# Performance work log

Hardware: AMD Instinct MI355X
Metric: run time of the kernel (lower is better)

## Reference

```python
import jax, jax.numpy as jnp
import numpy as np

B, S, H = 8, 1024, 768
NH, DH = 12, 64
F, E = 3072, 8
EPS = 1e-12

def layer_norm(x, g, b):
    mu = jnp.mean(x, axis=-1, keepdims=True)
    var = jnp.var(x, axis=-1, keepdims=True)
    return g * (x - mu) / jnp.sqrt(var + EPS) + b

def setup_inputs():
    key = jax.random.key(0)
    ks = jax.random.split(key, 20)
    std = 0.02
    d = {
        'hidden_states': jax.random.normal(ks[0], (B, S, H), jnp.float32),
        'Wq': jax.random.normal(ks[1], (H, H)) * std, 'bq': jnp.zeros((H,)),
        'Wk': jax.random.normal(ks[2], (H, H)) * std, 'bk': jnp.zeros((H,)),
        'Wv': jax.random.normal(ks[3], (H, H)) * std, 'bv': jnp.zeros((H,)),
        'Wao': jax.random.normal(ks[4], (H, H)) * std, 'bao': jnp.zeros((H,)),
        'ln1_g': jnp.ones((H,)), 'ln1_b': jnp.zeros((H,)),
        'Wr': jax.random.normal(ks[5], (H, E)) * std, 'br': jnp.zeros((E,)),
        'Wi': jax.random.normal(ks[6], (E, H, F)) * std, 'bi': jnp.zeros((E, F)),
        'Wo': jax.random.normal(ks[7], (F, H)) * std, 'bo': jnp.zeros((H,)),
        'ln2_g': jnp.ones((H,)), 'ln2_b': jnp.zeros((H,)),
    }
    return d

def reference(hidden_states, Wq, bq, Wk, bk, Wv, bv, Wao, bao, ln1_g, ln1_b,
              Wr, br, Wi, bi, Wo, bo, ln2_g, ln2_b):
    b, s, h = hidden_states.shape
    # --- self attention ---
    q = (hidden_states @ Wq + bq).reshape(b, s, NH, DH)
    k = (hidden_states @ Wk + bk).reshape(b, s, NH, DH)
    v = (hidden_states @ Wv + bv).reshape(b, s, NH, DH)
    scores = jnp.einsum('bqhd,bkhd->bhqk', q, k) / jnp.sqrt(jnp.float32(DH))
    probs = jax.nn.softmax(scores, axis=-1)
    ctx = jnp.einsum('bhqk,bkhd->bqhd', probs, v).reshape(b, s, h)
    attention_output = layer_norm(ctx @ Wao + bao + hidden_states, ln1_g, ln1_b)
    # --- router ---
    routing_scores = jax.nn.softmax(attention_output @ Wr + br, axis=-1)  # [b,s,E]
    routing_expert = jnp.argmax(routing_scores, axis=-1)  # [b,s]
    # --- expert FFN (dispatch/combine via per-expert masking) ---
    flat_x = attention_output.reshape(-1, h)          # [T,H]
    flat_e = routing_expert.reshape(-1)               # [T]
    flat_inter = jnp.zeros((b * s, F), flat_x.dtype)
    for e in range(E):
        mask = (flat_e == e)[:, None].astype(flat_x.dtype)
        y = jax.nn.gelu(flat_x @ Wi[e] + bi[e], approximate=False)
        flat_inter = flat_inter + mask * y
    inter = flat_inter.reshape(b, s, F)
    # --- output (dense + residual layernorm) ---
    layer_output = layer_norm(inter @ Wo + bo + attention_output, ln2_g, ln2_b)
    return layer_output, routing_scores
```

## Files before the change

kernel.cpp:

```cpp
#include <hip/hip_runtime.h>
#include <math.h>
#include <stdint.h>

#define TOKS 8192
#define HDIM 768
#define FDIM 3072
#define NEXP 8
#define NHEAD 12
#define SEQ 1024
#define BATCH 8
#define PERMSZ 9216

typedef __attribute__((ext_vector_type(8))) short s16x8;
typedef __attribute__((ext_vector_type(4))) short s16x4;
typedef __attribute__((ext_vector_type(4))) float f32x4;

__device__ __forceinline__ short f2bf(float f) {
  uint32_t u = __float_as_uint(f);
  uint32_t r = (u + 0x7fffu + ((u >> 16) & 1u)) >> 16;
  return (short)(r & 0xffffu);
}
__device__ __forceinline__ float bf2f(short h) {
  return __uint_as_float(((uint32_t)(uint16_t)h) << 16);
}
__device__ __forceinline__ void gload16(const void* g, void* l) {
  __builtin_amdgcn_global_load_lds(
      (const __attribute__((address_space(1))) uint32_t*)g,
      (__attribute__((address_space(3))) uint32_t*)l, 16, 0, 0);
}
__device__ __forceinline__ void pipe_wait_barrier() {
  asm volatile("s_waitcnt vmcnt(0)" ::: "memory");
  __builtin_amdgcn_s_barrier();
}

__global__ __launch_bounds__(256) void convert_split(
    const float* __restrict__ X, short* __restrict__ Xh, short* __restrict__ Xl, int n4)
{
  const int i = blockIdx.x * 256 + threadIdx.x;
  if (i >= n4) return;
  const float4 v = ((const float4*)X)[i];
  const float a[4] = {v.x, v.y, v.z, v.w};
  s16x4 h, l;
#pragma unroll
  for (int j = 0; j < 4; ++j) {
    h[j] = f2bf(a[j]);
    l[j] = f2bf(a[j] - bf2f(h[j]));
  }
  ((s16x4*)Xh)[i] = h;
  ((s16x4*)Xl)[i] = l;
}

__global__ __launch_bounds__(256) void transpose_split(
    const float* __restrict__ W, short* __restrict__ WTh, short* __restrict__ WTl,
    int K, int N)
{
  __shared__ float t[32][33];
  const int tid = threadIdx.x;
  const int tx = tid & 31, ty = tid >> 5;
  const int n0 = blockIdx.x * 32, k0 = blockIdx.y * 32;
#pragma unroll
  for (int r = 0; r < 4; ++r)
    t[ty + r * 8][tx] = W[(size_t)(k0 + ty + r * 8) * N + n0 + tx];
  __syncthreads();
#pragma unroll
  for (int r = 0; r < 4; ++r) {
    const float v = t[tx][ty + r * 8];
    const short h = f2bf(v);
    WTh[(size_t)(n0 + ty + r * 8) * K + k0 + tx] = h;
    WTl[(size_t)(n0 + ty + r * 8) * K + k0 + tx] = f2bf(v - bf2f(h));
  }
}

__global__ __launch_bounds__(256) void qkv_split_mfma(
    const short* __restrict__ Ah, const short* __restrict__ Al,
    const short* __restrict__ BhT, const short* __restrict__ BlT,
    const float* __restrict__ bias,
    short* __restrict__ QKh, short* __restrict__ QKl,
    short* __restrict__ VTh, short* __restrict__ VTl)
{
  const int K = 768;
  __shared__ __align__(16) short lAh[4096];
  __shared__ __align__(16) short lAl[4096];
  __shared__ __align__(16) short lBh[2][4096];
  __shared__ __align__(16) short lBl[2][4096];
  const int dsp = blockIdx.x + 18 * blockIdx.y;
  const int orig = (dsp & 7) * 144 + (dsp >> 3);
  const int bx = orig % 18, by = orig / 18;
  const int tid = threadIdx.x;
  const int w = tid >> 6, lane = tid & 63;
  const int wr = w >> 1, wc = w & 1;
  const int row0 = by * 128, col0 = bx * 128;
  const int sr = lane & 15, kg = lane >> 4;
  const size_t a0 = (size_t)(row0 + 2 * w * 16 + sr) * K + kg * 8;
  const size_t a1 = a0 + (size_t)16 * K;
  const size_t b0 = (size_t)(col0 + 2 * w * 16 + sr) * K + kg * 8;
  const size_t b1 = b0 + (size_t)16 * K;
  const int d0 = (2 * w) * 512, d1 = (2 * w + 1) * 512;
#define STAGE_QA(k0) do { \
    gload16(Ah + a0 + (k0), &lAh[d0]); \
    gload16(Ah + a1 + (k0), &lAh[d1]); \
    gload16(Al + a0 + (k0), &lAl[d0]); \
    gload16(Al + a1 + (k0), &lAl[d1]); \
  } while (0)
#define STAGE_QB(bu, k0) do { \
    gload16(BhT + b0 + (k0), &lBh[bu][d0]); \
    gload16(BhT + b1 + (k0), &lBh[bu][d1]); \
    gload16(BlT + b0 + (k0), &lBl[bu][d0]); \
    gload16(BlT + b1 + (k0), &lBl[bu][d1]); \
  } while (0)
  f32x4 acc[4][4] = {};
  STAGE_QA(0);
  STAGE_QB(0, 0);
  pipe_wait_barrier();
  int cur = 0;
  for (int t = 0; t < 24; ++t) {
    s16x8 ah[4], al[4], bh[4], bl[4];
#pragma unroll
    for (int i = 0; i < 4; ++i) {
      ah[i] = *(const s16x8*)&lAh[(wr * 4 + i) * 512 + lane * 8];
      al[i] = *(const s16x8*)&lAl[(wr * 4 + i) * 512 + lane * 8];
      bh[i] = *(const s16x8*)&lBh[cur][(wc * 4 + i) * 512 + lane * 8];
      bl[i] = *(const s16x8*)&lBl[cur][(wc * 4 + i) * 512 + lane * 8];
    }
    __syncthreads();
    if (t < 23) {
      STAGE_QA((t + 1) * 32);
      STAGE_QB(cur ^ 1, (t + 1) * 32);
    }
#pragma unroll
    for (int mi = 0; mi < 4; ++mi)
#pragma unroll
      for (int ni = 0; ni < 4; ++ni) {
        acc[mi][ni] = __builtin_amdgcn_mfma_f32_16x16x32_bf16(ah[mi], bh[ni], acc[mi][ni], 0, 0, 0);
        acc[mi][ni] = __builtin_amdgcn_mfma_f32_16x16x32_bf16(ah[mi], bl[ni], acc[mi][ni], 0, 0, 0);
        acc[mi][ni] = __builtin_amdgcn_mfma_f32_16x16x32_bf16(al[mi], bh[ni], acc[mi][ni], 0, 0, 0);
      }
    pipe_wait_barrier();
    cur ^= 1;
  }
#undef STAGE_QA
#undef STAGE_QB
  const int cl = lane & 15, rg = lane >> 4;
#pragma unroll
  for (int mi = 0; mi < 4; ++mi)
#pragma unroll
    for (int ni = 0; ni < 4; ++ni) {
      const int c = col0 + wc * 64 + ni * 16 + cl;
      const int rowb = row0 + wr * 64 + mi * 16 + rg * 4;
      const float qscale = (c < 768) ? 0.125f : 1.0f;
      s16x4 hv, lv;
#pragma unroll
      for (int r = 0; r < 4; ++r) {
        const float v = (acc[mi][ni][r] + bias[c]) * qscale;
        const short hh = f2bf(v);
        hv[r] = hh;
        lv[r] = f2bf(v - bf2f(hh));
      }
      if (c < 1536) {
#pragma unroll
        for (int r = 0; r < 4; ++r) {
          QKh[(size_t)(rowb + r) * 1536 + c] = hv[r];
          QKl[(size_t)(rowb + r) * 1536 + c] = lv[r];
        }
      } else {
        const int dall = c - 1536;
        const size_t vi = (((size_t)((rowb >> 10) * NHEAD + (dall >> 6))) * 64 + (dall & 63)) * 1024
                          + (rowb & 1023);
        *(s16x4*)(VTh + vi) = hv;
        *(s16x4*)(VTl + vi) = lv;
      }
    }
}

__global__ __launch_bounds__(256) void gemm_splitk_staged(
    const short* __restrict__ Ah, const short* __restrict__ Al,
    const short* __restrict__ BhT, const short* __restrict__ BlT,
    const float* __restrict__ bias, float* __restrict__ C0, float* __restrict__ C1,
    int N, int K)
{
  __shared__ __align__(16) short lAh[2][4096];
  __shared__ __align__(16) short lAl[2][4096];
  __shared__ __align__(16) short lBh[2][4096];
  __shared__ __align__(16) short lBl[2][4096];
  const int tid = threadIdx.x;
  const int w = tid >> 6, lane = tid & 63;
  const int wr = w >> 1, wc = w & 1;
  const int row0 = blockIdx.y * 128, col0 = blockIdx.x * 128;
  const int z = blockIdx.z;
  const int Khalf = K >> 1, koff = z * Khalf;
  const int sr = lane & 15, kg = lane >> 4;
  const size_t a0 = (size_t)(row0 + 2 * w * 16 + sr) * K + koff + kg * 8;
  const size_t a1 = a0 + (size_t)16 * K;
  const size_t b0 = (size_t)(col0 + 2 * w * 16 + sr) * K + koff + kg * 8;
  const size_t b1 = b0 + (size_t)16 * K;
  const int d0 = (2 * w) * 512, d1 = (2 * w + 1) * 512;
#define STAGE_K4(bu, k0) do { \
    gload16(Ah + a0 + (k0), &lAh[bu][d0]); \
    gload16(Ah + a1 + (k0), &lAh[bu][d1]); \
    gload16(Al + a0 + (k0), &lAl[bu][d0]); \
    gload16(Al + a1 + (k0), &lAl[bu][d1]); \
    gload16(BhT + b0 + (k0), &lBh[bu][d0]); \
    gload16(BhT + b1 + (k0), &lBh[bu][d1]); \
    gload16(BlT + b0 + (k0), &lBl[bu][d0]); \
    gload16(BlT + b1 + (k0), &lBl[bu][d1]); \
  } while (0)
  f32x4 acc[4][4] = {};
  const int NT = Khalf >> 5;
  STAGE_K4(0, 0);
  pipe_wait_barrier();
  int cur = 0;
  for (int t = 0; t < NT; ++t) {
    if (t + 1 < NT) STAGE_K4(cur ^ 1, (t + 1) * 32);
    s16x8 ah[4], al[4], bh[4], bl[4];
#pragma unroll
    for (int i = 0; i < 4; ++i) {
      ah[i] = *(const s16x8*)&lAh[cur][(wr * 4 + i) * 512 + lane * 8];
      al[i] = *(const s16x8*)&lAl[cur][(wr * 4 + i) * 512 + lane * 8];
      bh[i] = *(const s16x8*)&lBh[cur][(wc * 4 + i) * 512 + lane * 8];
      bl[i] = *(const s16x8*)&lBl[cur][(wc * 4 + i) * 512 + lane * 8];
    }
#pragma unroll
    for (int mi = 0; mi < 4; ++mi)
#pragma unroll
      for (int ni = 0; ni < 4; ++ni) {
        acc[mi][ni] = __builtin_amdgcn_mfma_f32_16x16x32_bf16(ah[mi], bh[ni], acc[mi][ni], 0, 0, 0);
        acc[mi][ni] = __builtin_amdgcn_mfma_f32_16x16x32_bf16(ah[mi], bl[ni], acc[mi][ni], 0, 0, 0);
        acc[mi][ni] = __builtin_amdgcn_mfma_f32_16x16x32_bf16(al[mi], bh[ni], acc[mi][ni], 0, 0, 0);
      }
    pipe_wait_barrier();
    cur ^= 1;
  }
#undef STAGE_K4
  float* C = z ? C1 : C0;
  const int cl = lane & 15, rg = lane >> 4;
#pragma unroll
  for (int mi = 0; mi < 4; ++mi)
#pragma unroll
    for (int r = 0; r < 4; ++r) {
      const int row = row0 + wr * 64 + mi * 16 + rg * 4 + r;
#pragma unroll
      for (int ni = 0; ni < 4; ++ni) {
        const int c = col0 + wc * 64 + ni * 16 + cl;
        C[(size_t)row * N + c] = acc[mi][ni][r] + (z ? 0.f : bias[c]);
      }
    }
}

__global__ __launch_bounds__(128, 2) void attention_part(
    const short* __restrict__ QKh, const short* __restrict__ QKl,
    const short* __restrict__ VTh, const short* __restrict__ VTl,
    float* __restrict__ O0, float* __restrict__ O1,
    float2* __restrict__ ml0, float2* __restrict__ ml1)
{
  __shared__ __align__(16) short lPh[2][2560];
  const int tid = threadIdx.x;
  const int w = tid >> 6, lane = tid & 63;
  const int dsp = blockIdx.x + 32 * (blockIdx.y + 12 * blockIdx.z);
  const int orig = (dsp & 7) * 384 + (dsp >> 3);
  const int wx = orig & 31;
  const int b = orig / 384, h = (orig >> 5) % 12;
  const int z = wx & 1;
  const int q0 = (wx >> 1) * 64 + w * 32;
  const int kv0 = z * 512;
  const int sr = lane & 15, kg = lane >> 4;
  const int cl = sr, rg = kg;
  short* myPh = lPh[w];
  float* Op = z ? O1 : O0;
  float2* mlp = z ? ml1 : ml0;

  s16x8 qh[2][2], ql[2][2];
  {
    const size_t qbase = ((size_t)b * SEQ + q0 + sr) * 1536 + h * 64 + kg * 8;
#pragma unroll
    for (int mi = 0; mi < 2; ++mi)
#pragma unroll
      for (int ks = 0; ks < 2; ++ks) {
        const size_t o = qbase + (size_t)mi * (16 * 1536) + ks * 32;
        qh[mi][ks] = *(const s16x8*)(QKh + o);
        ql[mi][ks] = *(const s16x8*)(QKl + o);
      }
  }
  float m_run[2][4], l_run[2][4];
#pragma unroll
  for (int mi = 0; mi < 2; ++mi)
#pragma unroll
    for (int r = 0; r < 4; ++r) { m_run[mi][r] = -3.0e38f; l_run[mi][r] = 0.f; }
  f32x4 acc_o[2][4] = {};

  for (int kt = kv0; kt < kv0 + 512; kt += 64) {
    s16x8 kh[4][2];
    {
      const size_t kbase = ((size_t)b * SEQ + kt + sr) * 1536 + 768 + h * 64 + kg * 8;
#pragma unroll
      for (int ni = 0; ni < 4; ++ni)
#pragma unroll
        for (int ks = 0; ks < 2; ++ks) {
          const size_t o = kbase + (size_t)ni * (16 * 1536) + ks * 32;
          kh[ni][ks] = *(const s16x8*)(QKh + o);
        }
    }
    f32x4 accs[2][4] = {};
    __builtin_amdgcn_s_setprio(1);
#pragma unroll
    for (int ks = 0; ks < 2; ++ks)
#pragma unroll
      for (int ni = 0; ni < 4; ++ni)
#pragma unroll
        for (int mi = 0; mi < 2; ++mi) {
          accs[mi][ni] = __builtin_amdgcn_mfma_f32_16x16x32_bf16(qh[mi][ks], kh[ni][ks], accs[mi][ni], 0, 0, 0);
          accs[mi][ni] = __builtin_amdgcn_mfma_f32_16x16x32_bf16(ql[mi][ks], kh[ni][ks], accs[mi][ni], 0, 0, 0);
        }
    __builtin_amdgcn_s_setprio(0);
    s16x8 vh[4][2], vl2[4][2];
    {
      const size_t vbase = (((size_t)(b * NHEAD + h)) * 64 + sr) * 1024 + kt + kg * 8;
#pragma unroll
      for (int nd = 0; nd < 4; ++nd)
#pragma unroll
        for (int ks2 = 0; ks2 < 2; ++ks2) {
          const size_t o = vbase + (size_t)nd * (16 * 1024) + ks2 * 32;
          vh[nd][ks2] = *(const s16x8*)(VTh + o);
          vl2[nd][ks2] = *(const s16x8*)(VTl + o);
        }
    }
#pragma unroll
    for (int mi = 0; mi < 2; ++mi)
#pragma unroll
      for (int r = 0; r < 4; ++r) {
        float mx = fmaxf(fmaxf(accs[mi][0][r], accs[mi][1][r]),
                         fmaxf(accs[mi][2][r], accs[mi][3][r]));
        mx = fmaxf(mx, __shfl_xor(mx, 1));
        mx = fmaxf(mx, __shfl_xor(mx, 2));
        mx = fmaxf(mx, __shfl_xor(mx, 4));
        mx = fmaxf(mx, __shfl_xor(mx, 8));
        const float mn = fmaxf(m_run[mi][r], mx);
        const float c = __expf(m_run[mi][r] - mn);
        m_run[mi][r] = mn;
        l_run[mi][r] *= c;
#pragma unroll
        for (int nd = 0; nd < 4; ++nd) acc_o[mi][nd][r] *= c;
        float sum = 0.f;
#pragma unroll
        for (int ni = 0; ni < 4; ++ni) {
          const float p = __expf(accs[mi][ni][r] - mn);
          const short hh = f2bf(p);
          sum += bf2f(hh);
          const int idx = (mi * 2 + (ni >> 1)) * 640 + (rg * 4 + r) * 40 + (ni & 1) * 16 + cl;
          myPh[idx] = hh;
        }
        sum += __shfl_xor(sum, 1);
        sum += __shfl_xor(sum, 2);
        sum += __shfl_xor(sum, 4);
        sum += __shfl_xor(sum, 8);
        l_run[mi][r] += sum;
      }
    __builtin_amdgcn_s_setprio(1);
#pragma unroll
    for (int ks2 = 0; ks2 < 2; ++ks2) {
      s16x8 pf[2];
#pragma unroll
      for (int mi = 0; mi < 2; ++mi) {
        const int ra = (mi * 2 + ks2) * 640 + sr * 40 + kg * 8;
        pf[mi] = *(const s16x8*)&myPh[ra];
      }
#pragma unroll
      for (int nd = 0; nd < 4; ++nd)
#pragma unroll
        for (int mi = 0; mi < 2; ++mi) {
          acc_o[mi][nd] = __builtin_amdgcn_mfma_f32_16x16x32_bf16(pf[mi], vh[nd][ks2], acc_o[mi][nd], 0, 0, 0);
          acc_o[mi][nd] = __builtin_amdgcn_mfma_f32_16x16x32_bf16(pf[mi], vl2[nd][ks2], acc_o[mi][nd], 0, 0, 0);
        }
    }
    __builtin_amdgcn_s_setprio(0);
  }
#pragma unroll
  for (int mi = 0; mi < 2; ++mi)
#pragma unroll
    for (int nd = 0; nd < 4; ++nd)
#pragma unroll
      for (int r = 0; r < 4; ++r) {
        const int row = q0 + mi * 16 + rg * 4 + r;
        const int d = h * 64 + nd * 16 + cl;
        Op[((size_t)b * SEQ + row) * HDIM + d] = acc_o[mi][nd][r];
      }
  if (sr == 0) {
#pragma unroll
    for (int mi = 0; mi < 2; ++mi)
#pragma unroll
      for (int r = 0; r < 4; ++r) {
        const int row = q0 + mi * 16 + rg * 4 + r;
        mlp[(size_t)(b * NHEAD + h) * SEQ + row] = make_float2(m_run[mi][r], l_run[mi][r]);
      }
  }
}

__global__ __launch_bounds__(256) void combine_split(
    const float* __restrict__ O0, const float* __restrict__ O1,
    const float2* __restrict__ ml0, const float2* __restrict__ ml1,
    short* __restrict__ Ch, short* __restrict__ Cl)
{
  const int t = blockIdx.x;
  const int b = t >> 10, s = t & 1023;
  const int tid = threadIdx.x;
#pragma unroll
  for (int i = 0; i < 3; ++i) {
    const int idx = tid + i * 256;
    const int h = idx >> 6;
    const float2 a0 = ml0[(size_t)(b * NHEAD + h) * SEQ + s];
    const float2 a1 = ml1[(size_t)(b * NHEAD + h) * SEQ + s];
    const float mm = fmaxf(a0.x, a1.x);
    const float w0 = __expf(a0.x - mm), w1 = __expf(a1.x - mm);
    const float denom = a0.y * w0 + a1.y * w1;
    const size_t o = (size_t)t * HDIM + idx;
    const float v = (O0[o] * w0 + O1[o] * w1) / denom;
    const short hh = f2bf(v);
    Ch[o] = hh;
    Cl[o] = f2bf(v - bf2f(hh));
  }
}

__global__ __launch_bounds__(256) void transpose_to_bf16(
    const float* __restrict__ W, short* __restrict__ WT, int K, int N)
{
  const size_t off = (size_t)blockIdx.z * (size_t)K * N;
  const float* Wp = W + off;
  short* WTp = WT + off;
  __shared__ float t[32][33];
  const int tid = threadIdx.x;
  const int tx = tid & 31, ty = tid >> 5;
  const int n0 = blockIdx.x * 32, k0 = blockIdx.y * 32;
#pragma unroll
  for (int r = 0; r < 4; ++r)
    t[ty + r * 8][tx] = Wp[(size_t)(k0 + ty + r * 8) * N + n0 + tx];
  __syncthreads();
#pragma unroll
  for (int r = 0; r < 4; ++r)
    WTp[(size_t)(n0 + ty + r * 8) * K + k0 + tx] = f2bf(t[tx][ty + r * 8]);
}

__global__ __launch_bounds__(256) void expert_up_mfma(
    const short* __restrict__ Abf, const short* __restrict__ WiT,
    const float* __restrict__ bi, const int* __restrict__ perm,
    const int* __restrict__ offs, short* __restrict__ interb)
{
  const int row0 = blockIdx.x * 128;
  if (row0 >= offs[NEXP]) return;
  int e = 0;
  while (offs[e + 1] <= row0) ++e;
  __shared__ __align__(16) short lA[2][4096];
  __shared__ __align__(16) short lB[2][4096];
  __shared__ int toks[128];
  const int tid = threadIdx.x;
  const int w = tid >> 6, lane = tid & 63;
  const int wr = w >> 1, wc = w & 1;
  const int col0 = blockIdx.y * 128;
  if (tid < 128) toks[tid] = perm[row0 + tid];
  __syncthreads();
  const int sr = lane & 15, kg = lane >> 4;
  int t0 = toks[2 * w * 16 + sr];        if (t0 < 0) t0 = toks[0];
  int t1 = toks[(2 * w + 1) * 16 + sr];  if (t1 < 0) t1 = toks[0];
  const size_t a0 = (size_t)t0 * HDIM + kg * 8;
  const size_t a1 = (size_t)t1 * HDIM + kg * 8;
  const short* Bt = WiT + (size_t)e * FDIM * HDIM;
  const size_t b0 = (size_t)(col0 + 2 * w * 16 + sr) * HDIM + kg * 8;
  const size_t b1 = b0 + (size_t)16 * HDIM;
  const int d0 = (2 * w) * 512, d1 = (2 * w + 1) * 512;
#define STAGE_E(bu, k0) do { \
    gload16(Abf + a0 + (k0), &lA[bu][d0]); \
    gload16(Abf + a1 + (k0), &lA[bu][d1]); \
    gload16(Bt + b0 + (k0), &lB[bu][d0]); \
    gload16(Bt + b1 + (k0), &lB[bu][d1]); \
  } while (0)
  f32x4 acc[4][4] = {};
  STAGE_E(0, 0);
  pipe_wait_barrier();
  int cur = 0;
  for (int t = 0; t < 24; ++t) {
    if (t < 23) STAGE_E(cur ^ 1, (t + 1) * 32);
    s16x8 af[4], bg[4];
#pragma unroll
    for (int i = 0; i < 4; ++i) {
      af[i] = *(const s16x8*)&lA[cur][(wr * 4 + i) * 512 + lane * 8];
      bg[i] = *(const s16x8*)&lB[cur][(wc * 4 + i) * 512 + lane * 8];
    }
#pragma unroll
    for (int mi = 0; mi < 4; ++mi)
#pragma unroll
      for (int ni = 0; ni < 4; ++ni)
        acc[mi][ni] = __builtin_amdgcn_mfma_f32_16x16x32_bf16(af[mi], bg[ni], acc[mi][ni], 0, 0, 0);
    pipe_wait_barrier();
    cur ^= 1;
  }
#undef STAGE_E
  const int cl = lane & 15, rg = lane >> 4;
#pragma unroll
  for (int mi = 0; mi < 4; ++mi) {
#pragma unroll
    for (int r = 0; r < 4; ++r) {
      const int rl = wr * 64 + mi * 16 + rg * 4 + r;
      const int tok = toks[rl];
      if (tok < 0) continue;
#pragma unroll
      for (int ni = 0; ni < 4; ++ni) {
        const int c = col0 + wc * 64 + ni * 16 + cl;
        float v = acc[mi][ni][r] + bi[(size_t)e * FDIM + c];
        v = 0.5f * v * (1.0f + erff(v * 0.70710678118654752f));
        interb[(size_t)tok * FDIM + c] = f2bf(v);
      }
    }
  }
}

__global__ __launch_bounds__(256) void wo_mfma(
    const short* __restrict__ Ab, const short* __restrict__ BT,
    const float* __restrict__ bias, float* __restrict__ C0, float* __restrict__ C1)
{
  __shared__ __align__(16) short lA[2][4096];
  __shared__ __align__(16) short lB[2][4096];
  const int tid = threadIdx.x;
  const int w = tid >> 6, lane = tid & 63;
  const int wr = w >> 1, wc = w & 1;
  const int row0 = blockIdx.y * 128, col0 = blockIdx.x * 128;
  const int z = blockIdx.z;
  const int kbase = z * 1536;
  const int sr = lane & 15, kg = lane >> 4;
  const size_t a0 = (size_t)(row0 + 2 * w * 16 + sr) * FDIM + kbase + kg * 8;
  const size_t a1 = a0 + (size_t)16 * FDIM;
  const size_t b0 = (size_t)(col0 + 2 * w * 16 + sr) * FDIM + kbase + kg * 8;
  const size_t b1 = b0 + (size_t)16 * FDIM;
  const int d0 = (2 * w) * 512, d1 = (2 * w + 1) * 512;
#define STAGE_W(bu, k0) do { \
    gload16(Ab + a0 + (k0), &lA[bu][d0]); \
    gload16(Ab + a1 + (k0), &lA[bu][d1]); \
    gload16(BT + b0 + (k0), &lB[bu][d0]); \
    gload16(BT + b1 + (k0), &lB[bu][d1]); \
  } while (0)
  f32x4 acc[4][4] = {};
  STAGE_W(0, 0);
  pipe_wait_barrier();
  int cur = 0;
  for (int t = 0; t < 48; ++t) {
    if (t < 47) STAGE_W(cur ^ 1, (t + 1) * 32);
    s16x8 af[4], bg[4];
#pragma unroll
    for (int i = 0; i < 4; ++i) {
      af[i] = *(const s16x8*)&lA[cur][(wr * 4 + i) * 512 + lane * 8];
      bg[i] = *(const s16x8*)&lB[cur][(wc * 4 + i) * 512 + lane * 8];
    }
#pragma unroll
    for (int mi = 0; mi < 4; ++mi)
#pragma unroll
      for (int ni = 0; ni < 4; ++ni)
        acc[mi][ni] = __builtin_amdgcn_mfma_f32_16x16x32_bf16(af[mi], bg[ni], acc[mi][ni], 0, 0, 0);
    pipe_wait_barrier();
    cur ^= 1;
  }
#undef STAGE_W
  float* C = z ? C1 : C0;
  const int cl = lane & 15, rg = lane >> 4;
#pragma unroll
  for (int mi = 0; mi < 4; ++mi) {
#pragma unroll
    for (int r = 0; r < 4; ++r) {
      const int row = row0 + wr * 64 + mi * 16 + rg * 4 + r;
#pragma unroll
      for (int ni = 0; ni < 4; ++ni) {
        const int c = col0 + wc * 64 + ni * 16 + cl;
        C[(size_t)row * HDIM + c] = acc[mi][ni][r] + (z ? 0.f : bias[c]);
      }
    }
  }
}

__global__ __launch_bounds__(256) void add2_ln_kernel(
    const float* __restrict__ X1, const float* __restrict__ X2,
    const float* __restrict__ R, const float* __restrict__ g,
    const float* __restrict__ bb, float* __restrict__ out)
{
  const int t = blockIdx.x;
  const int tid = threadIdx.x;
  const float* x1 = X1 + (size_t)t * HDIM;
  const float* x2 = X2 + (size_t)t * HDIM;
  const float* r = R + (size_t)t * HDIM;
  float v[3];
  float sum = 0.f, ssq = 0.f;
#pragma unroll
  for (int i = 0; i < 3; ++i) {
    const float val = x1[tid + i * 256] + x2[tid + i * 256] + r[tid + i * 256];
    v[i] = val;
    sum += val;
    ssq += val * val;
  }
#pragma unroll
  for (int o = 32; o > 0; o >>= 1) {
    sum += __shfl_down(sum, o);
    ssq += __shfl_down(ssq, o);
  }
  __shared__ float red[10];
  const int wid = tid >> 6, lane = tid & 63;
  if (lane == 0) { red[wid] = sum; red[4 + wid] = ssq; }
  __syncthreads();
  if (tid == 0) {
    const float s = red[0] + red[1] + red[2] + red[3];
    const float q = red[4] + red[5] + red[6] + red[7];
    const float mean = s * (1.f / HDIM);
    const float var = q * (1.f / HDIM) - mean * mean;
    red[8] = mean;
    red[9] = rsqrtf(fmaxf(var, 0.f) + 1e-12f);
  }
  __syncthreads();
  const float mean = red[8], rstd = red[9];
#pragma unroll
  for (int i = 0; i < 3; ++i) {
    const int idx = tid + i * 256;
    out[(size_t)t * HDIM + idx] = g[idx] * (v[i] - mean) * rstd + bb[idx];
  }
}

__global__ __launch_bounds__(256) void add2_ln_bf16_kernel(
    const float* __restrict__ X1, const float* __restrict__ X2,
    const float* __restrict__ R, const float* __restrict__ g,
    const float* __restrict__ bb, float* __restrict__ out, short* __restrict__ outb)
{
  const int t = blockIdx.x;
  const int tid = threadIdx.x;
  const float* x1 = X1 + (size_t)t * HDIM;
  const float* x2 = X2 + (size_t)t * HDIM;
  const float* r = R + (size_t)t * HDIM;
  float v[3];
  float sum = 0.f, ssq = 0.f;
#pragma unroll
  for (int i = 0; i < 3; ++i) {
    const float val = x1[tid + i * 256] + x2[tid + i * 256] + r[tid + i * 256];
    v[i] = val;
    sum += val;
    ssq += val * val;
  }
#pragma unroll
  for (int o = 32; o > 0; o >>= 1) {
    sum += __shfl_down(sum, o);
    ssq += __shfl_down(ssq, o);
  }
  __shared__ float red[10];
  const int wid = tid >> 6, lane = tid & 63;
  if (lane == 0) { red[wid] = sum; red[4 + wid] = ssq; }
  __syncthreads();
  if (tid == 0) {
    const float s = red[0] + red[1] + red[2] + red[3];
    const float q = red[4] + red[5] + red[6] + red[7];
    const float mean = s * (1.f / HDIM);
    const float var = q * (1.f / HDIM) - mean * mean;
    red[8] = mean;
    red[9] = rsqrtf(fmaxf(var, 0.f) + 1e-12f);
  }
  __syncthreads();
  const float mean = red[8], rstd = red[9];
#pragma unroll
  for (int i = 0; i < 3; ++i) {
    const int idx = tid + i * 256;
    const float o = g[idx] * (v[i] - mean) * rstd + bb[idx];
    out[(size_t)t * HDIM + idx] = o;
    outb[(size_t)t * HDIM + idx] = f2bf(o);
  }
}

__global__ __launch_bounds__(256) void router_kernel(
    const float* __restrict__ X, const float* __restrict__ Wr,
    const float* __restrict__ br, float* __restrict__ scores_out,
    int* __restrict__ expert, int* __restrict__ counts)
{
  const int wid = threadIdx.x >> 6, lane = threadIdx.x & 63;
  const int tok = blockIdx.x * 4 + wid;
  const float* x = X + (size_t)tok * HDIM;
  float acc[8] = {};
  for (int k0 = 0; k0 < HDIM; k0 += 64) {
    const float xv = x[k0 + lane];
    const float* wrow = Wr + (size_t)(k0 + lane) * NEXP;
    const float4 w0 = *reinterpret_cast<const float4*>(wrow);
    const float4 w1 = *reinterpret_cast<const float4*>(wrow + 4);
    acc[0] = fmaf(xv, w0.x, acc[0]);
    acc[1] = fmaf(xv, w0.y, acc[1]);
    acc[2] = fmaf(xv, w0.z, acc[2]);
    acc[3] = fmaf(xv, w0.w, acc[3]);
    acc[4] = fmaf(xv, w1.x, acc[4]);
    acc[5] = fmaf(xv, w1.y, acc[5]);
    acc[6] = fmaf(xv, w1.z, acc[6]);
    acc[7] = fmaf(xv, w1.w, acc[7]);
  }
#pragma unroll
  for (int e = 0; e < 8; ++e)
#pragma unroll
    for (int o = 32; o > 0; o >>= 1) acc[e] += __shfl_down(acc[e], o);
  if (lane == 0) {
    float mx = -3.0e38f;
#pragma unroll
    for (int e = 0; e < 8; ++e) { acc[e] += br[e]; mx = fmaxf(mx, acc[e]); }
    float sum = 0.f;
#pragma unroll
    for (int e = 0; e < 8; ++e) { acc[e] = expf(acc[e] - mx); sum += acc[e]; }
    const float inv = 1.f / sum;
    int best = 0;
    float bv = acc[0];
#pragma unroll
    for (int e = 0; e < 8; ++e) {
      const float p = acc[e] * inv;
      scores_out[(size_t)tok * NEXP + e] = p;
      if (acc[e] > bv) { bv = acc[e]; best = e; }
    }
    expert[tok] = best;
    atomicAdd(&counts[best], 1);
  }
}

__global__ void offsets_kernel(const int* __restrict__ counts, int* __restrict__ offs)
{
  if (threadIdx.x == 0 && blockIdx.x == 0) {
    int a = 0;
    for (int e = 0; e < NEXP; ++e) {
      offs[e] = a;
      a += ((counts[e] + 127) >> 7) << 7;
    }
    offs[NEXP] = a;
  }
}

__global__ __launch_bounds__(256) void scatter_kernel(
    const int* __restrict__ expert, const int* __restrict__ offs,
    int* __restrict__ cursor, int* __restrict__ perm)
{
  const int t = blockIdx.x * 256 + threadIdx.x;
  if (t >= TOKS) return;
  const int e = expert[t];
  const int pos = atomicAdd(&cursor[e], 1);
  perm[offs[e] + pos] = t;
}

extern "C" void kernel_launch(void* const* d_in, const int* in_sizes, int n_in,
                              void* d_out, int out_size, void* d_ws, size_t ws_size,
                              hipStream_t stream) {
  const float* hidden = (const float*)d_in[0];
  const float* Wq  = (const float*)d_in[1];
  const float* bq  = (const float*)d_in[2];
  const float* Wk  = (const float*)d_in[3];
  const float* bk  = (const float*)d_in[4];
  const float* Wv  = (const float*)d_in[5];
  const float* bv  = (const float*)d_in[6];
  const float* Wao = (const float*)d_in[7];
  const float* bao = (const float*)d_in[8];
  const float* ln1g = (const float*)d_in[9];
  const float* ln1b = (const float*)d_in[10];
  const float* Wr  = (const float*)d_in[11];
  const float* br  = (const float*)d_in[12];
  const float* Wi  = (const float*)d_in[13];
  const float* bi  = (const float*)d_in[14];
  const float* Wo  = (const float*)d_in[15];
  const float* bo  = (const float*)d_in[16];
  const float* ln2g = (const float*)d_in[17];
  const float* ln2b = (const float*)d_in[18];

  float* out = (float*)d_out;
  float* scores_out = out + (size_t)TOKS * HDIM;

  const size_t M1 = (size_t)TOKS * HDIM;
  const size_t HW = (size_t)HDIM * HDIM;
  float* ws = (float*)d_ws;
  short* QKhb = (short*)ws;
  short* QKlb = (short*)(ws + M1);
  short* VThb = (short*)(ws + 2 * M1);
  short* VTlb = VThb + (size_t)BATCH * NHEAD * 64 * 1024;
  float* O0b  = ws + 3 * M1;
  float* O1b  = ws + 4 * M1;
  float* bqkv = ws + 3 * M1;
  short* Hh = (short*)(ws + 4 * M1);
  short* Hl = Hh + M1;
  short* Ch = (short*)(ws + 2 * M1);
  short* Cl = Ch + M1;
  short* wt = (short*)(ws + 5 * M1);
  short* WqkvhT = wt;
  short* WqkvlT = wt + 3 * HW;
  short* WaohT  = wt + 6 * HW;
  short* WaolT  = wt + 7 * HW;
  float2* ml0 = (float2*)(ws + 5 * M1 + 4 * HW);
  float2* ml1 = ml0 + (size_t)BATCH * NHEAD * SEQ;
  float* aoproj0  = ws;
  float* aoproj1  = ws + 3 * M1;
  float* attn_out = ws + M1;
  float* tmp2a    = ws;
  float* tmp2b    = ws + 3 * M1;
  short* Abf    = (short*)(ws + 2 * M1);
  short* WiT    = Abf + M1;
  short* WoT    = WiT + (size_t)NEXP * FDIM * HDIM;
  short* interb = WoT + (size_t)HDIM * FDIM;
  int* ints   = (int*)(interb + (size_t)TOKS * FDIM);
  int* perm   = ints;
  int* expert = ints + PERMSZ;
  int* counts = expert + TOKS;
  int* offs   = counts + NEXP;
  int* cursor = offs + NEXP + 1;

  hipMemsetAsync(counts, 0, (NEXP + NEXP + 1 + NEXP) * sizeof(int), stream);
  hipMemsetAsync(perm, 0xFF, PERMSZ * sizeof(int), stream);
  hipMemcpyAsync(bqkv,        bq, HDIM * sizeof(float), hipMemcpyDeviceToDevice, stream);
  hipMemcpyAsync(bqkv + 768,  bk, HDIM * sizeof(float), hipMemcpyDeviceToDevice, stream);
  hipMemcpyAsync(bqkv + 1536, bv, HDIM * sizeof(float), hipMemcpyDeviceToDevice, stream);

  const dim3 blk(256);
  convert_split<<<dim3(TOKS * HDIM / 4 / 256), blk, 0, stream>>>(hidden, Hh, Hl, TOKS * HDIM / 4);
  transpose_split<<<dim3(24, 24), blk, 0, stream>>>(Wq,  WqkvhT,          WqkvlT,          HDIM, HDIM);
  transpose_split<<<dim3(24, 24), blk, 0, stream>>>(Wk,  WqkvhT + HW,     WqkvlT + HW,     HDIM, HDIM);
  transpose_split<<<dim3(24, 24), blk, 0, stream>>>(Wv,  WqkvhT + 2 * HW, WqkvlT + 2 * HW, HDIM, HDIM);
  transpose_split<<<dim3(24, 24), blk, 0, stream>>>(Wao, WaohT,           WaolT,           HDIM, HDIM);

  qkv_split_mfma<<<dim3(2304 / 128, TOKS / 128), blk, 0, stream>>>(
      Hh, Hl, WqkvhT, WqkvlT, bqkv, QKhb, QKlb, VThb, VTlb);

  attention_part<<<dim3((SEQ / 64) * 2, NHEAD, BATCH), dim3(128), 0, stream>>>(
      QKhb, QKlb, VThb, VTlb, O0b, O1b, ml0, ml1);
  combine_split<<<dim3(TOKS), blk, 0, stream>>>(O0b, O1b, ml0, ml1, Ch, Cl);

  gemm_splitk_staged<<<dim3(HDIM / 128, TOKS / 128, 2), blk, 0, stream>>>(
      Ch, Cl, WaohT, WaolT, bao, aoproj0, aoproj1, HDIM, HDIM);
  add2_ln_bf16_kernel<<<dim3(TOKS), blk, 0, stream>>>(
      aoproj0, aoproj1, hidden, ln1g, ln1b, attn_out, Abf);

  router_kernel<<<dim3(TOKS / 4), blk, 0, stream>>>(attn_out, Wr, br, scores_out, expert, counts);
  offsets_kernel<<<dim3(1), dim3(64), 0, stream>>>(counts, offs);
  scatter_kernel<<<dim3(TOKS / 256), blk, 0, stream>>>(expert, offs, cursor, perm);

  transpose_to_bf16<<<dim3(FDIM / 32, HDIM / 32, NEXP), blk, 0, stream>>>(Wi, WiT, HDIM, FDIM);
  transpose_to_bf16<<<dim3(HDIM / 32, FDIM / 32, 1), blk, 0, stream>>>(Wo, WoT, FDIM, HDIM);

  expert_up_mfma<<<dim3(PERMSZ / 128, FDIM / 128), blk, 0, stream>>>(
      Abf, WiT, bi, perm, offs, interb);
  wo_mfma<<<dim3(HDIM / 128, TOKS / 128, 2), blk, 0, stream>>>(interb, WoT, bo, tmp2a, tmp2b);
  add2_ln_kernel<<<dim3(TOKS), blk, 0, stream>>>(tmp2a, tmp2b, attn_out, ln2g, ln2b, out);
}
```

Measured before the change: 810.2 us.

## Single-buffer LDS tiles in GEMM kernels with register-staged prefetch

Replaces the double-buffered LDS tiles in the QKV, split-K, expert FFN and Wo GEMM kernels with single buffers. Each iteration now loads fragments into registers, synchronizes, then issues the next tile's global-to-LDS loads before running the MFMAs. This halves LDS use per block so more blocks can be resident per CU. The cost is an extra barrier per iteration and less slack between the next tile's load and its use.

```diff
diff --git a/kernel.cpp b/kernel.cpp
--- a/kernel.cpp
+++ b/kernel.cpp
@@ -81,8 +81,8 @@
   const int K = 768;
   __shared__ __align__(16) short lAh[4096];
   __shared__ __align__(16) short lAl[4096];
-  __shared__ __align__(16) short lBh[2][4096];
-  __shared__ __align__(16) short lBl[2][4096];
+  __shared__ __align__(16) short lBh[4096];
+  __shared__ __align__(16) short lBl[4096];
   const int dsp = blockIdx.x + 18 * blockIdx.y;
   const int orig = (dsp & 7) * 144 + (dsp >> 3);
   const int bx = orig % 18, by = orig / 18;
@@ -96,37 +96,30 @@
   const size_t b0 = (size_t)(col0 + 2 * w * 16 + sr) * K + kg * 8;
   const size_t b1 = b0 + (size_t)16 * K;
   const int d0 = (2 * w) * 512, d1 = (2 * w + 1) * 512;
-#define STAGE_QA(k0) do { \
+#define STAGE_Q(k0) do { \
     gload16(Ah + a0 + (k0), &lAh[d0]); \
     gload16(Ah + a1 + (k0), &lAh[d1]); \
     gload16(Al + a0 + (k0), &lAl[d0]); \
     gload16(Al + a1 + (k0), &lAl[d1]); \
-  } while (0)
-#define STAGE_QB(bu, k0) do { \
-    gload16(BhT + b0 + (k0), &lBh[bu][d0]); \
-    gload16(BhT + b1 + (k0), &lBh[bu][d1]); \
-    gload16(BlT + b0 + (k0), &lBl[bu][d0]); \
-    gload16(BlT + b1 + (k0), &lBl[bu][d1]); \
+    gload16(BhT + b0 + (k0), &lBh[d0]); \
+    gload16(BhT + b1 + (k0), &lBh[d1]); \
+    gload16(BlT + b0 + (k0), &lBl[d0]); \
+    gload16(BlT + b1 + (k0), &lBl[d1]); \
   } while (0)
   f32x4 acc[4][4] = {};
-  STAGE_QA(0);
-  STAGE_QB(0, 0);
+  STAGE_Q(0);
   pipe_wait_barrier();
-  int cur = 0;
   for (int t = 0; t < 24; ++t) {
     s16x8 ah[4], al[4], bh[4], bl[4];
 #pragma unroll
     for (int i = 0; i < 4; ++i) {
       ah[i] = *(const s16x8*)&lAh[(wr * 4 + i) * 512 + lane * 8];
       al[i] = *(const s16x8*)&lAl[(wr * 4 + i) * 512 + lane * 8];
-      bh[i] = *(const s16x8*)&lBh[cur][(wc * 4 + i) * 512 + lane * 8];
-      bl[i] = *(const s16x8*)&lBl[cur][(wc * 4 + i) * 512 + lane * 8];
+      bh[i] = *(const s16x8*)&lBh[(wc * 4 + i) * 512 + lane * 8];
+      bl[i] = *(const s16x8*)&lBl[(wc * 4 + i) * 512 + lane * 8];
     }
     __syncthreads();
-    if (t < 23) {
-      STAGE_QA((t + 1) * 32);
-      STAGE_QB(cur ^ 1, (t + 1) * 32);
-    }
+    if (t < 23) STAGE_Q((t + 1) * 32);
 #pragma unroll
     for (int mi = 0; mi < 4; ++mi)
 #pragma unroll
@@ -136,10 +129,8 @@
         acc[mi][ni] = __builtin_amdgcn_mfma_f32_16x16x32_bf16(al[mi], bh[ni], acc[mi][ni], 0, 0, 0);
       }
     pipe_wait_barrier();
-    cur ^= 1;
-  }
-#undef STAGE_QA
-#undef STAGE_QB
+  }
+#undef STAGE_Q
   const int cl = lane & 15, rg = lane >> 4;
 #pragma unroll
   for (int mi = 0; mi < 4; ++mi)
@@ -178,10 +169,10 @@
     const float* __restrict__ bias, float* __restrict__ C0, float* __restrict__ C1,
     int N, int K)
 {
-  __shared__ __align__(16) short lAh[2][4096];
-  __shared__ __align__(16) short lAl[2][4096];
-  __shared__ __align__(16) short lBh[2][4096];
-  __shared__ __align__(16) short lBl[2][4096];
+  __shared__ __align__(16) short lAh[4096];
+  __shared__ __align__(16) short lAl[4096];
+  __shared__ __align__(16) short lBh[4096];
+  __shared__ __align__(16) short lBl[4096];
   const int tid = threadIdx.x;
   const int w = tid >> 6, lane = tid & 63;
   const int wr = w >> 1, wc = w & 1;
@@ -194,31 +185,31 @@
   const size_t b0 = (size_t)(col0 + 2 * w * 16 + sr) * K + koff + kg * 8;
   const size_t b1 = b0 + (size_t)16 * K;
   const int d0 = (2 * w) * 512, d1 = (2 * w + 1) * 512;
-#define STAGE_K4(bu, k0) do { \
-    gload16(Ah + a0 + (k0), &lAh[bu][d0]); \
-    gload16(Ah + a1 + (k0), &lAh[bu][d1]); \
-    gload16(Al + a0 + (k0), &lAl[bu][d0]); \
-    gload16(Al + a1 + (k0), &lAl[bu][d1]); \
-    gload16(BhT + b0 + (k0), &lBh[bu][d0]); \
-    gload16(BhT + b1 + (k0), &lBh[bu][d1]); \
-    gload16(BlT + b0 + (k0), &lBl[bu][d0]); \
-    gload16(BlT + b1 + (k0), &lBl[bu][d1]); \
+#define STAGE_K4(k0) do { \
+    gload16(Ah + a0 + (k0), &lAh[d0]); \
+    gload16(Ah + a1 + (k0), &lAh[d1]); \
+    gload16(Al + a0 + (k0), &lAl[d0]); \
+    gload16(Al + a1 + (k0), &lAl[d1]); \
+    gload16(BhT + b0 + (k0), &lBh[d0]); \
+    gload16(BhT + b1 + (k0), &lBh[d1]); \
+    gload16(BlT + b0 + (k0), &lBl[d0]); \
+    gload16(BlT + b1 + (k0), &lBl[d1]); \
   } while (0)
   f32x4 acc[4][4] = {};
   const int NT = Khalf >> 5;
-  STAGE_K4(0, 0);
+  STAGE_K4(0);
   pipe_wait_barrier();
-  int cur = 0;
   for (int t = 0; t < NT; ++t) {
-    if (t + 1 < NT) STAGE_K4(cur ^ 1, (t + 1) * 32);
     s16x8 ah[4], al[4], bh[4], bl[4];
 #pragma unroll
     for (int i = 0; i < 4; ++i) {
-      ah[i] = *(const s16x8*)&lAh[cur][(wr * 4 + i) * 512 + lane * 8];
-      al[i] = *(const s16x8*)&lAl[cur][(wr * 4 + i) * 512 + lane * 8];
-      bh[i] = *(const s16x8*)&lBh[cur][(wc * 4 + i) * 512 + lane * 8];
-      bl[i] = *(const s16x8*)&lBl[cur][(wc * 4 + i) * 512 + lane * 8];
-    }
+      ah[i] = *(const s16x8*)&lAh[(wr * 4 + i) * 512 + lane * 8];
+      al[i] = *(const s16x8*)&lAl[(wr * 4 + i) * 512 + lane * 8];
+      bh[i] = *(const s16x8*)&lBh[(wc * 4 + i) * 512 + lane * 8];
+      bl[i] = *(const s16x8*)&lBl[(wc * 4 + i) * 512 + lane * 8];
+    }
+    __syncthreads();
+    if (t + 1 < NT) STAGE_K4((t + 1) * 32);
 #pragma unroll
     for (int mi = 0; mi < 4; ++mi)
 #pragma unroll
@@ -228,7 +219,6 @@
         acc[mi][ni] = __builtin_amdgcn_mfma_f32_16x16x32_bf16(al[mi], bh[ni], acc[mi][ni], 0, 0, 0);
       }
     pipe_wait_barrier();
-    cur ^= 1;
   }
 #undef STAGE_K4
   float* C = z ? C1 : C0;
@@ -447,8 +437,8 @@
   if (row0 >= offs[NEXP]) return;
   int e = 0;
   while (offs[e + 1] <= row0) ++e;
-  __shared__ __align__(16) short lA[2][4096];
-  __shared__ __align__(16) short lB[2][4096];
+  __shared__ __align__(16) short lA[4096];
+  __shared__ __align__(16) short lB[4096];
   __shared__ int toks[128];
   const int tid = threadIdx.x;
   const int w = tid >> 6, lane = tid & 63;
@@ -465,31 +455,30 @@
   const size_t b0 = (size_t)(col0 + 2 * w * 16 + sr) * HDIM + kg * 8;
   const size_t b1 = b0 + (size_t)16 * HDIM;
   const int d0 = (2 * w) * 512, d1 = (2 * w + 1) * 512;
-#define STAGE_E(bu, k0) do { \
-    gload16(Abf + a0 + (k0), &lA[bu][d0]); \
-    gload16(Abf + a1 + (k0), &lA[bu][d1]); \
-    gload16(Bt + b0 + (k0), &lB[bu][d0]); \
-    gload16(Bt + b1 + (k0), &lB[bu][d1]); \
+#define STAGE_E(k0) do { \
+    gload16(Abf + a0 + (k0), &lA[d0]); \
+    gload16(Abf + a1 + (k0), &lA[d1]); \
+    gload16(Bt + b0 + (k0), &lB[d0]); \
+    gload16(Bt + b1 + (k0), &lB[d1]); \
   } while (0)
   f32x4 acc[4][4] = {};
-  STAGE_E(0, 0);
+  STAGE_E(0);
   pipe_wait_barrier();
-  int cur = 0;
   for (int t = 0; t < 24; ++t) {
-    if (t < 23) STAGE_E(cur ^ 1, (t + 1) * 32);
     s16x8 af[4], bg[4];
 #pragma unroll
     for (int i = 0; i < 4; ++i) {
-      af[i] = *(const s16x8*)&lA[cur][(wr * 4 + i) * 512 + lane * 8];
-      bg[i] = *(const s16x8*)&lB[cur][(wc * 4 + i) * 512 + lane * 8];
-    }
+      af[i] = *(const s16x8*)&lA[(wr * 4 + i) * 512 + lane * 8];
+      bg[i] = *(const s16x8*)&lB[(wc * 4 + i) * 512 + lane * 8];
+    }
+    __syncthreads();
+    if (t < 23) STAGE_E((t + 1) * 32);
 #pragma unroll
     for (int mi = 0; mi < 4; ++mi)
 #pragma unroll
       for (int ni = 0; ni < 4; ++ni)
         acc[mi][ni] = __builtin_amdgcn_mfma_f32_16x16x32_bf16(af[mi], bg[ni], acc[mi][ni], 0, 0, 0);
     pipe_wait_barrier();
-    cur ^= 1;
   }
 #undef STAGE_E
   const int cl = lane & 15, rg = lane >> 4;
@@ -515,8 +504,8 @@
     const short* __restrict__ Ab, const short* __restrict__ BT,
     const float* __restrict__ bias, float* __restrict__ C0, float* __restrict__ C1)
 {
-  __shared__ __align__(16) short lA[2][4096];
-  __shared__ __align__(16) short lB[2][4096];
+  __shared__ __align__(16) short lA[4096];
+  __shared__ __align__(16) short lB[4096];
   const int tid = threadIdx.x;
   const int w = tid >> 6, lane = tid & 63;
   const int wr = w >> 1, wc = w & 1;
@@ -529,31 +518,30 @@
   const size_t b0 = (size_t)(col0 + 2 * w * 16 + sr) * FDIM + kbase + kg * 8;
   const size_t b1 = b0 + (size_t)16 * FDIM;
   const int d0 = (2 * w) * 512, d1 = (2 * w + 1) * 512;
-#define STAGE_W(bu, k0) do { \
-    gload16(Ab + a0 + (k0), &lA[bu][d0]); \
-    gload16(Ab + a1 + (k0), &lA[bu][d1]); \
-    gload16(BT + b0 + (k0), &lB[bu][d0]); \
-    gload16(BT + b1 + (k0), &lB[bu][d1]); \
+#define STAGE_W(k0) do { \
+    gload16(Ab + a0 + (k0), &lA[d0]); \
+    gload16(Ab + a1 + (k0), &lA[d1]); \
+    gload16(BT + b0 + (k0), &lB[d0]); \
+    gload16(BT + b1 + (k0), &lB[d1]); \
   } while (0)
   f32x4 acc[4][4] = {};
-  STAGE_W(0, 0);
+  STAGE_W(0);
   pipe_wait_barrier();
-  int cur = 0;
   for (int t = 0; t < 48; ++t) {
-    if (t < 47) STAGE_W(cur ^ 1, (t + 1) * 32);
     s16x8 af[4], bg[4];
 #pragma unroll
     for (int i = 0; i < 4; ++i) {
-      af[i] = *(const s16x8*)&lA[cur][(wr * 4 + i) * 512 + lane * 8];
-      bg[i] = *(const s16x8*)&lB[cur][(wc * 4 + i) * 512 + lane * 8];
-    }
+      af[i] = *(const s16x8*)&lA[(wr * 4 + i) * 512 + lane * 8];
+      bg[i] = *(const s16x8*)&lB[(wc * 4 + i) * 512 + lane * 8];
+    }
+    __syncthreads();
+    if (t < 47) STAGE_W((t + 1) * 32);
 #pragma unroll
     for (int mi = 0; mi < 4; ++mi)
 #pragma unroll
       for (int ni = 0; ni < 4; ++ni)
         acc[mi][ni] = __builtin_amdgcn_mfma_f32_16x16x32_bf16(af[mi], bg[ni], acc[mi][ni], 0, 0, 0);
     pipe_wait_barrier();
-    cur ^= 1;
   }
 #undef STAGE_W
   float* C = z ? C1 : C0;
```

After: 798.9 us. Within noise of the previous version (-1.4%).

## Prefetch two K-tiles ahead in GEMM kernels with partial vmcnt waits

Applied to the files above, without the earlier changes.

Restructures the double-buffered GEMM loops (QKV, split-K, expert FFN, output dense) so two K-tiles are in flight. The buffer just read is refilled with tile t+2 after an LDS-read barrier, and each iteration waits only for the older tile through a partial vmcnt count. This hides more global-load latency than the previous one-tile lookahead. The QKV kernel now double-buffers the A operand too, which raises LDS use, and correctness depends on the vmcnt counts matching the number of loads per stage.

```diff
diff --git a/kernel.cpp b/kernel.cpp
--- a/kernel.cpp
+++ b/kernel.cpp
@@ -32,6 +32,10 @@
   asm volatile("s_waitcnt vmcnt(0)" ::: "memory");
   __builtin_amdgcn_s_barrier();
 }
+__device__ __forceinline__ void lds_read_barrier() {
+  asm volatile("s_waitcnt lgkmcnt(0)" ::: "memory");
+  __builtin_amdgcn_s_barrier();
+}
 
 __global__ __launch_bounds__(256) void convert_split(
     const float* __restrict__ X, short* __restrict__ Xh, short* __restrict__ Xl, int n4)
@@ -79,8 +83,8 @@
     short* __restrict__ VTh, short* __restrict__ VTl)
 {
   const int K = 768;
-  __shared__ __align__(16) short lAh[4096];
-  __shared__ __align__(16) short lAl[4096];
+  __shared__ __align__(16) short lAh[2][4096];
+  __shared__ __align__(16) short lAl[2][4096];
   __shared__ __align__(16) short lBh[2][4096];
   __shared__ __align__(16) short lBl[2][4096];
   const int dsp = blockIdx.x + 18 * blockIdx.y;
@@ -96,37 +100,33 @@
   const size_t b0 = (size_t)(col0 + 2 * w * 16 + sr) * K + kg * 8;
   const size_t b1 = b0 + (size_t)16 * K;
   const int d0 = (2 * w) * 512, d1 = (2 * w + 1) * 512;
-#define STAGE_QA(k0) do { \
-    gload16(Ah + a0 + (k0), &lAh[d0]); \
-    gload16(Ah + a1 + (k0), &lAh[d1]); \
-    gload16(Al + a0 + (k0), &lAl[d0]); \
-    gload16(Al + a1 + (k0), &lAl[d1]); \
-  } while (0)
-#define STAGE_QB(bu, k0) do { \
+#define STAGE_Q(bu, k0) do { \
+    gload16(Ah + a0 + (k0), &lAh[bu][d0]); \
+    gload16(Ah + a1 + (k0), &lAh[bu][d1]); \
+    gload16(Al + a0 + (k0), &lAl[bu][d0]); \
+    gload16(Al + a1 + (k0), &lAl[bu][d1]); \
     gload16(BhT + b0 + (k0), &lBh[bu][d0]); \
     gload16(BhT + b1 + (k0), &lBh[bu][d1]); \
     gload16(BlT + b0 + (k0), &lBl[bu][d0]); \
     gload16(BlT + b1 + (k0), &lBl[bu][d1]); \
   } while (0)
   f32x4 acc[4][4] = {};
-  STAGE_QA(0);
-  STAGE_QB(0, 0);
-  pipe_wait_barrier();
-  int cur = 0;
+  STAGE_Q(0, 0);
+  STAGE_Q(1, 32);
+  asm volatile("s_waitcnt vmcnt(8)" ::: "memory");
+  __builtin_amdgcn_s_barrier();
   for (int t = 0; t < 24; ++t) {
+    const int cur = t & 1;
     s16x8 ah[4], al[4], bh[4], bl[4];
 #pragma unroll
     for (int i = 0; i < 4; ++i) {
-      ah[i] = *(const s16x8*)&lAh[(wr * 4 + i) * 512 + lane * 8];
-      al[i] = *(const s16x8*)&lAl[(wr * 4 + i) * 512 + lane * 8];
+      ah[i] = *(const s16x8*)&lAh[cur][(wr * 4 + i) * 512 + lane * 8];
+      al[i] = *(const s16x8*)&lAl[cur][(wr * 4 + i) * 512 + lane * 8];
       bh[i] = *(const s16x8*)&lBh[cur][(wc * 4 + i) * 512 + lane * 8];
       bl[i] = *(const s16x8*)&lBl[cur][(wc * 4 + i) * 512 + lane * 8];
     }
-    __syncthreads();
-    if (t < 23) {
-      STAGE_QA((t + 1) * 32);
-      STAGE_QB(cur ^ 1, (t + 1) * 32);
-    }
+    lds_read_barrier();
+    if (t + 2 < 24) STAGE_Q(cur, (t + 2) * 32);
 #pragma unroll
     for (int mi = 0; mi < 4; ++mi)
 #pragma unroll
@@ -135,11 +135,11 @@
         acc[mi][ni] = __builtin_amdgcn_mfma_f32_16x16x32_bf16(ah[mi], bl[ni], acc[mi][ni], 0, 0, 0);
         acc[mi][ni] = __builtin_amdgcn_mfma_f32_16x16x32_bf16(al[mi], bh[ni], acc[mi][ni], 0, 0, 0);
       }
-    pipe_wait_barrier();
-    cur ^= 1;
-  }
-#undef STAGE_QA
-#undef STAGE_QB
+    if (t + 2 < 24) asm volatile("s_waitcnt vmcnt(8)" ::: "memory");
+    else            asm volatile("s_waitcnt vmcnt(0)" ::: "memory");
+    __builtin_amdgcn_s_barrier();
+  }
+#undef STAGE_Q
   const int cl = lane & 15, rg = lane >> 4;
 #pragma unroll
   for (int mi = 0; mi < 4; ++mi)
@@ -207,10 +207,11 @@
   f32x4 acc[4][4] = {};
   const int NT = Khalf >> 5;
   STAGE_K4(0, 0);
-  pipe_wait_barrier();
-  int cur = 0;
+  STAGE_K4(1, 32);
+  asm volatile("s_waitcnt vmcnt(8)" ::: "memory");
+  __builtin_amdgcn_s_barrier();
   for (int t = 0; t < NT; ++t) {
-    if (t + 1 < NT) STAGE_K4(cur ^ 1, (t + 1) * 32);
+    const int cur = t & 1;
     s16x8 ah[4], al[4], bh[4], bl[4];
 #pragma unroll
     for (int i = 0; i < 4; ++i) {
@@ -219,6 +220,8 @@
       bh[i] = *(const s16x8*)&lBh[cur][(wc * 4 + i) * 512 + lane * 8];
       bl[i] = *(const s16x8*)&lBl[cur][(wc * 4 + i) * 512 + lane * 8];
     }
+    lds_read_barrier();
+    if (t + 2 < NT) STAGE_K4(cur, (t + 2) * 32);
 #pragma unroll
     for (int mi = 0; mi < 4; ++mi)
 #pragma unroll
@@ -227,8 +230,9 @@
         acc[mi][ni] = __builtin_amdgcn_mfma_f32_16x16x32_bf16(ah[mi], bl[ni], acc[mi][ni], 0, 0, 0);
         acc[mi][ni] = __builtin_amdgcn_mfma_f32_16x16x32_bf16(al[mi], bh[ni], acc[mi][ni], 0, 0, 0);
       }
-    pipe_wait_barrier();
-    cur ^= 1;
+    if (t + 2 < NT) asm volatile("s_waitcnt vmcnt(8)" ::: "memory");
+    else            asm volatile("s_waitcnt vmcnt(0)" ::: "memory");
+    __builtin_amdgcn_s_barrier();
   }
 #undef STAGE_K4
   float* C = z ? C1 : C0;
@@ -473,23 +477,27 @@
   } while (0)
   f32x4 acc[4][4] = {};
   STAGE_E(0, 0);
-  pipe_wait_barrier();
-  int cur = 0;
+  STAGE_E(1, 32);
+  asm volatile("s_waitcnt vmcnt(4)" ::: "memory");
+  __builtin_amdgcn_s_barrier();
   for (int t = 0; t < 24; ++t) {
-    if (t < 23) STAGE_E(cur ^ 1, (t + 1) * 32);
+    const int cur = t & 1;
     s16x8 af[4], bg[4];
 #pragma unroll
     for (int i = 0; i < 4; ++i) {
       af[i] = *(const s16x8*)&lA[cur][(wr * 4 + i) * 512 + lane * 8];
       bg[i] = *(const s16x8*)&lB[cur][(wc * 4 + i) * 512 + lane * 8];
     }
+    lds_read_barrier();
+    if (t + 2 < 24) STAGE_E(cur, (t + 2) * 32);
 #pragma unroll
     for (int mi = 0; mi < 4; ++mi)
 #pragma unroll
       for (int ni = 0; ni < 4; ++ni)
         acc[mi][ni] = __builtin_amdgcn_mfma_f32_16x16x32_bf16(af[mi], bg[ni], acc[mi][ni], 0, 0, 0);
-    pipe_wait_barrier();
-    cur ^= 1;
+    if (t + 2 < 24) asm volatile("s_waitcnt vmcnt(4)" ::: "memory");
+    else            asm volatile("s_waitcnt vmcnt(0)" ::: "memory");
+    __builtin_amdgcn_s_barrier();
   }
 #undef STAGE_E
   const int cl = lane & 15, rg = lane >> 4;
@@ -537,23 +545,27 @@
   } while (0)
   f32x4 acc[4][4] = {};
   STAGE_W(0, 0);
-  pipe_wait_barrier();
-  int cur = 0;
+  STAGE_W(1, 32);
+  asm volatile("s_waitcnt vmcnt(4)" ::: "memory");
+  __builtin_amdgcn_s_barrier();
   for (int t = 0; t < 48; ++t) {
-    if (t < 47) STAGE_W(cur ^ 1, (t + 1) * 32);
+    const int cur = t & 1;
     s16x8 af[4], bg[4];
 #pragma unroll
     for (int i = 0; i < 4; ++i) {
       af[i] = *(const s16x8*)&lA[cur][(wr * 4 + i) * 512 + lane * 8];
       bg[i] = *(const s16x8*)&lB[cur][(wc * 4 + i) * 512 + lane * 8];
     }
+    lds_read_barrier();
+    if (t + 2 < 48) STAGE_W(cur, (t + 2) * 32);
 #pragma unroll
     for (int mi = 0; mi < 4; ++mi)
 #pragma unroll
       for (int ni = 0; ni < 4; ++ni)
         acc[mi][ni] = __builtin_amdgcn_mfma_f32_16x16x32_bf16(af[mi], bg[ni], acc[mi][ni], 0, 0, 0);
-    pipe_wait_barrier();
-    cur ^= 1;
+    if (t + 2 < 48) asm volatile("s_waitcnt vmcnt(4)" ::: "memory");
+    else            asm volatile("s_waitcnt vmcnt(0)" ::: "memory");
+    __builtin_amdgcn_s_barrier();
   }
 #undef STAGE_W
   float* C = z ? C1 : C0;
```

After: 832.1 us. 1.03x slower.
